# Performance work log

Measured on AMD Instinct MI355X. Metric: run time of the kernel, lower is better.

## Reference

```python
import jax, jax.numpy as jnp
import numpy as np


def setup_inputs() -> dict:
    key = jax.random.key(0)
    ks = jax.random.split(key, 5)
    B, TOTAL_IN, GROUPS, IN_NUM, OUT = 500000, 200, 25, 8, 75
    x = jax.random.normal(ks[0], (B, TOTAL_IN), dtype=jnp.float32)
    w1 = jax.random.normal(ks[1], (IN_NUM, 1), dtype=jnp.float32) * 0.35
    b1 = jax.random.normal(ks[2], (1,), dtype=jnp.float32) * 0.1
    w2 = jax.random.normal(ks[3], (1, 3), dtype=jnp.float32) * 0.5
    b2 = jax.random.normal(ks[4], (3,), dtype=jnp.float32) * 0.1
    # in_out_map: 25 groups, each gathers 8 input cols and scatters 3 output cols
    in_out_k = jnp.arange(GROUPS * IN_NUM, dtype=jnp.int32).reshape(GROUPS, IN_NUM)
    in_out_v = jnp.arange(GROUPS * 3, dtype=jnp.int32).reshape(GROUPS, 3)
    return {"x": x, "w1": w1, "b1": b1, "w2": w2, "b2": b2,
            "in_out_k": in_out_k, "in_out_v": in_out_v}


def reference(x, w1, b1, w2, b2, in_out_k, in_out_v):
    B = x.shape[0]
    OUT = 75
    # Batched gather of all groups at once: [B, G, IN_NUM]
    g = x[:, in_out_k]
    # Shared tiny MLP applied to every group: Linear(IN_NUM,1) -> ReLU -> Linear(1,3)
    h = jax.nn.relu(jnp.einsum('bgi,io->bgo', g, w1) + b1)   # [B, G, 1]
    o = jnp.einsum('bgo,ot->bgt', h, w2) + b2                 # [B, G, 3]
    # Scatter group outputs into the [B, 75] output (zeros elsewhere)
    out = jnp.zeros((B, OUT), dtype=x.dtype)
    out = out.at[:, in_out_v.reshape(-1)].set(o.reshape(B, -1))
    return out
```

## Files before the change

kernel.cpp:

```cpp
#include <hip/hip_runtime.h>


#define GROUPS  25
#define IN_NUM  8
#define ROW     200
#define OUTROW  75
#define OUTT    3
#define RPB     32
#define THREADS 256

__global__ __launch_bounds__(THREADS) void mlp_rsna6_kernel(
    const float* __restrict__ x,
    const float* __restrict__ w1,
    const float* __restrict__ b1,
    const float* __restrict__ w2,
    const float* __restrict__ b2,
    const int*   __restrict__ iok,
    const int*   __restrict__ iov,
    float*       __restrict__ out,
    int nrows)
{
    __shared__ float xs[RPB * ROW];
    __shared__ float os[RPB * OUTROW];
    __shared__ int   kb_s[GROUPS];
    __shared__ int   vb_s[GROUPS];

    const int tid = threadIdx.x;
    const int r0  = blockIdx.x * RPB;
    const int rows = min(RPB, nrows - r0);

    if (tid < GROUPS) {
        kb_s[tid] = iok[tid * IN_NUM];
        vb_s[tid] = iov[tid * OUTT];
    }

    const float4* xg  = reinterpret_cast<const float4*>(x + (size_t)r0 * ROW);
    float4*       xs4 = reinterpret_cast<float4*>(xs);
    const int n4 = rows * (ROW / 4);
    for (int i = tid; i < n4; i += THREADS) xs4[i] = xg[i];

    const float W10 = w1[0], W11 = w1[1], W12 = w1[2], W13 = w1[3];
    const float W14 = w1[4], W15 = w1[5], W16 = w1[6], W17 = w1[7];
    const float B1  = b1[0];
    const float W20 = w2[0], W21 = w2[1], W22 = w2[2];
    const float B20 = b2[0], B21 = b2[1], B22 = b2[2];

    __syncthreads();

    const int items = rows * GROUPS;
    for (int i = tid; i < items; i += THREADS) {
        int bl = i / GROUPS;
        int g  = i - bl * GROUPS;
        int kb = kb_s[g];
        int vb = vb_s[g];

        const float4* xp = reinterpret_cast<const float4*>(&xs[bl * ROW + kb]);
        float4 a0 = xp[0];
        float4 a1 = xp[1];

        float s = B1;
        s = fmaf(a0.x, W10, s);
        s = fmaf(a0.y, W11, s);
        s = fmaf(a0.z, W12, s);
        s = fmaf(a0.w, W13, s);
        s = fmaf(a1.x, W14, s);
        s = fmaf(a1.y, W15, s);
        s = fmaf(a1.z, W16, s);
        s = fmaf(a1.w, W17, s);
        float h = fmaxf(s, 0.0f);

        float* op = &os[bl * OUTROW + vb];
        op[0] = fmaf(h, W20, B20);
        op[1] = fmaf(h, W21, B21);
        op[2] = fmaf(h, W22, B22);
    }

    __syncthreads();

    float4*       og  = reinterpret_cast<float4*>(out + (size_t)r0 * OUTROW);
    const float4* os4 = reinterpret_cast<const float4*>(os);
    const int fl  = rows * OUTROW;
    const int m4  = fl / 4;
    for (int i = tid; i < m4; i += THREADS) og[i] = os4[i];
    for (int i = m4 * 4 + tid; i < fl; i += THREADS)
        out[(size_t)r0 * OUTROW + i] = os[i];
}

extern "C" void kernel_launch(void* const* d_in, const int* in_sizes, int n_in,
                              void* d_out, int out_size, void* d_ws, size_t ws_size,
                              hipStream_t stream) {
    const float* x   = (const float*)d_in[0];
    const float* w1  = (const float*)d_in[1];
    const float* b1  = (const float*)d_in[2];
    const float* w2  = (const float*)d_in[3];
    const float* b2  = (const float*)d_in[4];
    const int*   iok = (const int*)d_in[5];
    const int*   iov = (const int*)d_in[6];
    float*       out = (float*)d_out;

    int nrows = in_sizes[0] / ROW;
    int grid  = (nrows + RPB - 1) / RPB;
    mlp_rsna6_kernel<<<grid, THREADS, 0, stream>>>(
        x, w1, b1, w2, b2, iok, iov, out, nrows);
}
```

Baseline: 568.6 us.

## Read inputs directly from global memory in persistent grid-stride blocks with double-buffered output

Drops the shared-memory staging of each 32-row input tile, so each thread loads its group's 8 floats straight from global memory. Blocks become persistent: a fixed grid walks tiles with a grid stride, and the output staging buffer alternates between two shared slots so only one barrier is needed per tile. Launch bounds now request higher occupancy. The aim is to cut LDS traffic and barriers and raise occupancy on a kernel limited by memory bandwidth. The cost is uncoalesced float4 loads at a 200-float row stride, which may hurt the efficiency of global reads.

```diff
diff --git a/kernel.cpp b/kernel.cpp
--- a/kernel.cpp
+++ b/kernel.cpp
@@ -9,7 +9,7 @@
 #define RPB     32
 #define THREADS 256
 
-__global__ __launch_bounds__(THREADS) void mlp_rsna6_kernel(
+__global__ __launch_bounds__(THREADS, 8) void mlp_rsna6_kernel(
     const float* __restrict__ x,
     const float* __restrict__ w1,
     const float* __restrict__ b1,
@@ -20,24 +20,17 @@
     float*       __restrict__ out,
     int nrows)
 {
-    __shared__ float xs[RPB * ROW];
-    __shared__ float os[RPB * OUTROW];
+    __shared__ float os[2][RPB * OUTROW];
     __shared__ int   kb_s[GROUPS];
     __shared__ int   vb_s[GROUPS];
 
     const int tid = threadIdx.x;
-    const int r0  = blockIdx.x * RPB;
-    const int rows = min(RPB, nrows - r0);
 
     if (tid < GROUPS) {
         kb_s[tid] = iok[tid * IN_NUM];
         vb_s[tid] = iov[tid * OUTT];
     }
-
-    const float4* xg  = reinterpret_cast<const float4*>(x + (size_t)r0 * ROW);
-    float4*       xs4 = reinterpret_cast<float4*>(xs);
-    const int n4 = rows * (ROW / 4);
-    for (int i = tid; i < n4; i += THREADS) xs4[i] = xg[i];
+    __syncthreads();
 
     const float W10 = w1[0], W11 = w1[1], W12 = w1[2], W13 = w1[3];
     const float W14 = w1[4], W15 = w1[5], W16 = w1[6], W17 = w1[7];
@@ -45,45 +38,52 @@
     const float W20 = w2[0], W21 = w2[1], W22 = w2[2];
     const float B20 = b2[0], B21 = b2[1], B22 = b2[2];
 
-    __syncthreads();
+    const int ntiles = (nrows + RPB - 1) / RPB;
+    int p = 0;
 
-    const int items = rows * GROUPS;
-    for (int i = tid; i < items; i += THREADS) {
-        int bl = i / GROUPS;
-        int g  = i - bl * GROUPS;
-        int kb = kb_s[g];
-        int vb = vb_s[g];
+    for (int t = blockIdx.x; t < ntiles; t += gridDim.x, p ^= 1) {
+        const int r0   = t * RPB;
+        const int rows = min(RPB, nrows - r0);
+        const int items = rows * GROUPS;
 
-        const float4* xp = reinterpret_cast<const float4*>(&xs[bl * ROW + kb]);
-        float4 a0 = xp[0];
-        float4 a1 = xp[1];
+        const float* xbase = x + (size_t)r0 * ROW;
 
-        float s = B1;
-        s = fmaf(a0.x, W10, s);
-        s = fmaf(a0.y, W11, s);
-        s = fmaf(a0.z, W12, s);
-        s = fmaf(a0.w, W13, s);
-        s = fmaf(a1.x, W14, s);
-        s = fmaf(a1.y, W15, s);
-        s = fmaf(a1.z, W16, s);
-        s = fmaf(a1.w, W17, s);
-        float h = fmaxf(s, 0.0f);
+        for (int i = tid; i < items; i += THREADS) {
+            int bl = i / GROUPS;
+            int g  = i - bl * GROUPS;
 
-        float* op = &os[bl * OUTROW + vb];
-        op[0] = fmaf(h, W20, B20);
-        op[1] = fmaf(h, W21, B21);
-        op[2] = fmaf(h, W22, B22);
+            const float4* xp = reinterpret_cast<const float4*>(
+                xbase + bl * ROW + kb_s[g]);
+            float4 a0 = xp[0];
+            float4 a1 = xp[1];
+
+            float s = B1;
+            s = fmaf(a0.x, W10, s);
+            s = fmaf(a0.y, W11, s);
+            s = fmaf(a0.z, W12, s);
+            s = fmaf(a0.w, W13, s);
+            s = fmaf(a1.x, W14, s);
+            s = fmaf(a1.y, W15, s);
+            s = fmaf(a1.z, W16, s);
+            s = fmaf(a1.w, W17, s);
+            float h = fmaxf(s, 0.0f);
+
+            float* op = &os[p][bl * OUTROW + vb_s[g]];
+            op[0] = fmaf(h, W20, B20);
+            op[1] = fmaf(h, W21, B21);
+            op[2] = fmaf(h, W22, B22);
+        }
+
+        __syncthreads();
+
+        float4*       og = reinterpret_cast<float4*>(out + (size_t)r0 * OUTROW);
+        const float4* s4 = reinterpret_cast<const float4*>(os[p]);
+        const int fl = rows * OUTROW;
+        const int m4 = fl / 4;
+        for (int i = tid; i < m4; i += THREADS) og[i] = s4[i];
+        for (int i = m4 * 4 + tid; i < fl; i += THREADS)
+            out[(size_t)r0 * OUTROW + i] = os[p][i];
     }
-
-    __syncthreads();
-
-    float4*       og  = reinterpret_cast<float4*>(out + (size_t)r0 * OUTROW);
-    const float4* os4 = reinterpret_cast<const float4*>(os);
-    const int fl  = rows * OUTROW;
-    const int m4  = fl / 4;
-    for (int i = tid; i < m4; i += THREADS) og[i] = os4[i];
-    for (int i = m4 * 4 + tid; i < fl; i += THREADS)
-        out[(size_t)r0 * OUTROW + i] = os[i];
 }
 
 extern "C" void kernel_launch(void* const* d_in, const int* in_sizes, int n_in,
@@ -99,7 +99,7 @@
     float*       out = (float*)d_out;
 
     int nrows = in_sizes[0] / ROW;
-    int grid  = (nrows + RPB - 1) / RPB;
+    int grid  = 2048;
     mlp_rsna6_kernel<<<grid, THREADS, 0, stream>>>(
         x, w1, b1, w2, b2, iok, iov, out, nrows);
 }
```

After: 569.7 us. No clear change (+0.2%).
